# Kernel tuning notes

Hardware: AMD Instinct MI355X
Metric: run time of the kernel (lower is better)

## Reference

```python
import jax, jax.numpy as jnp
import numpy as np


def setup_inputs() -> dict:
    key = jax.random.key(0)
    k1, k2, k3, k4 = jax.random.split(key, 4)
    B, C, H, W = 8, 256, 64, 64
    x = jax.random.normal(k1, (B, C, H, W), dtype=jnp.float32)
    wq = jax.random.normal(k2, (1, C), dtype=jnp.float32) * (1.0 / np.sqrt(C))
    wk = jax.random.normal(k3, (1, C), dtype=jnp.float32) * (1.0 / np.sqrt(C))
    wv = jax.random.normal(k4, (C, C), dtype=jnp.float32) * (1.0 / np.sqrt(C))
    gamma = jnp.zeros((1,), dtype=jnp.float32)
    return {"x": x, "wq": wq, "wk": wk, "wv": wv, "gamma": gamma}


def reference(x, wq, wk, wv, gamma):
    B, C, H, W = x.shape
    N = H * W
    xf = x.reshape(B, C, N)                      # [B, C, N]
    # 1x1 convs == channel matmuls
    f = jnp.einsum('oc,bcn->bon', wq, xf)        # [B, 1, N]
    g = jnp.einsum('oc,bcn->bon', wk, xf)        # [B, 1, N]
    h = jnp.einsum('oc,bcn->bon', wv, xf)        # [B, C, N]
    # scores[b, i, j] = f[b, 0, i] * g[b, 0, j]  -> [B, N, N]
    scores = jnp.einsum('bi,bj->bij', f[:, 0, :], g[:, 0, :])
    # softmax over dim=1 (rows), matching torch F.softmax(..., dim=1)
    beta = jax.nn.softmax(scores, axis=1)        # [B, N, N]
    gam = gamma[0]
    o = (1.0 - gam) * jnp.einsum('bcn,bnm->bcm', h, beta) + gam * xf
    return o.reshape(B, C, H, W)
```

## Files before the change

### kernel.cpp

```cpp
#include <hip/hip_runtime.h>
#include <math.h>

#define BQ 8
#define CQ 256
#define NQ 4096
#define MT 128
#define NSTEP (NQ / 32)

typedef short s16x8 __attribute__((ext_vector_type(8)));
typedef short s16x4 __attribute__((ext_vector_type(4)));
typedef float f32x4 __attribute__((ext_vector_type(4)));

static __device__ __forceinline__ float4 ld4(const float* p) { return *(const float4*)p; }

static constexpr float LOG2E = 1.4426950408889634f;

static __device__ __forceinline__ short f2bf(float f) {
    return __builtin_bit_cast(short, (__bf16)f);
}

__global__ void k_fg(const float* __restrict__ x, const float* __restrict__ wq,
                     const float* __restrict__ wk, float* __restrict__ fs,
                     float* __restrict__ g, short* __restrict__ xbf) {
    int b = blockIdx.y;
    int n = blockIdx.x * 256 + threadIdx.x;
    const float* xb = x + (size_t)b * CQ * NQ + n;
    short* xo = xbf + (size_t)b * CQ * NQ + n;
    float accf = 0.f, accg = 0.f;
#pragma unroll 8
    for (int c = 0; c < CQ; ++c) {
        float v = xb[(size_t)c * NQ];
        accf = fmaf(wq[c], v, accf);
        accg = fmaf(wk[c], v, accg);
        xo[(size_t)c * NQ] = f2bf(v);
    }
    fs[b * NQ + n] = accf * LOG2E;
    g[b * NQ + n]  = accg;
}

__global__ void k_minmax(const float* __restrict__ fs, float* __restrict__ fmx,
                         float* __restrict__ fmn) {
    int b = blockIdx.x;
    const float* f = fs + b * NQ;
    float mx = -1e30f, mn = 1e30f;
    for (int i = threadIdx.x; i < NQ; i += 256) {
        float v = f[i];
        mx = fmaxf(mx, v);
        mn = fminf(mn, v);
    }
    for (int off = 32; off; off >>= 1) {
        mx = fmaxf(mx, __shfl_down(mx, off));
        mn = fminf(mn, __shfl_down(mn, off));
    }
    __shared__ float smx[4], smn[4];
    int wid = threadIdx.x >> 6;
    if ((threadIdx.x & 63) == 0) { smx[wid] = mx; smn[wid] = mn; }
    __syncthreads();
    if (threadIdx.x == 0) {
        mx = fmaxf(fmaxf(smx[0], smx[1]), fmaxf(smx[2], smx[3]));
        mn = fminf(fminf(smn[0], smn[1]), fminf(smn[2], smn[3]));
        fmx[b] = mx;
        fmn[b] = mn;
    }
}

__global__ void __launch_bounds__(512, 2) k_attn(
    const short* __restrict__ xbf, const float* __restrict__ fsp,
    const float* __restrict__ gp, const float* __restrict__ fmxs,
    const float* __restrict__ fmns, const float* __restrict__ wv,
    const float* __restrict__ x, const float* __restrict__ gamma,
    float* __restrict__ out) {
    __shared__ __align__(16) char smem[65536];

    int bid = blockIdx.x;
    int b = bid & 7;
    int mblk = bid >> 3;
    int m0 = mblk * MT;
    int tid = threadIdx.x;
    int l = tid & 63;
    int w = tid >> 6;
    int wc = w & 1;
    int wm = w >> 1;
    int q = l >> 4;
    int cr = l & 15;

    float fmx = fmxs[b], fmn = fmns[b];
    const float* gb = gp + b * NQ;
    float gj[2], nM[2], zac[2];
#pragma unroll
    for (int jm = 0; jm < 2; ++jm) {
        float gv = gb[m0 + wm * 32 + jm * 16 + cr];
        gj[jm] = gv;
        nM[jm] = -((gv >= 0.f) ? gv * fmx : gv * fmn);
        zac[jm] = 0.f;
    }

    const float* fb = fsp + b * NQ;
    const short* xb = xbf + (size_t)b * CQ * NQ;

    f32x4 acc[8][2];
#pragma unroll
    for (int jc = 0; jc < 8; ++jc)
#pragma unroll
        for (int jm = 0; jm < 2; ++jm) acc[jc][jm] = (f32x4){0.f, 0.f, 0.f, 0.f};

#pragma unroll
    for (int r2 = 0; r2 < 2; ++r2) {
        int off = tid * 16 + r2 * 8192;
        int row = off >> 6, nb = off & 63;
        const short* src = xb + (size_t)row * NQ + (nb >> 1);
        __builtin_amdgcn_global_load_lds(
            (const __attribute__((address_space(1))) void*)src,
            (__attribute__((address_space(3))) void*)(smem + off), 16, 0, 0);
    }
    float4 fqa = *(const float4*)(fb + q * 8);
    float4 fqb = *(const float4*)(fb + q * 8 + 4);
    __syncthreads();

    for (int t = 0; t < NSTEP; ++t) {
        const char* cbuf = smem + (t & 1) * 16384;
        int n0n = ((t + 1) & (NSTEP - 1)) * 32;
        if (t + 1 < NSTEP) {
            char* nbuf = smem + ((t + 1) & 1) * 16384;
#pragma unroll
            for (int r2 = 0; r2 < 2; ++r2) {
                int off = tid * 16 + r2 * 8192;
                int row = off >> 6, nb = off & 63;
                const short* src = xb + (size_t)row * NQ + n0n + (nb >> 1);
                __builtin_amdgcn_global_load_lds(
                    (const __attribute__((address_space(1))) void*)src,
                    (__attribute__((address_space(3))) void*)(nbuf + off), 16, 0, 0);
            }
        }
        float4 fqa_n = *(const float4*)(fb + n0n + q * 8);
        float4 fqb_n = *(const float4*)(fb + n0n + q * 8 + 4);
        float fq[8] = {fqa.x, fqa.y, fqa.z, fqa.w, fqb.x, fqb.y, fqb.z, fqb.w};
        s16x8 bv[2];
#pragma unroll
        for (int jm = 0; jm < 2; ++jm) {
            float z = zac[jm];
#pragma unroll
            for (int i = 0; i < 8; ++i) {
                float e = __builtin_amdgcn_exp2f(fmaf(fq[i], gj[jm], nM[jm]));
                z += e;
                bv[jm][i] = f2bf(e);
            }
            zac[jm] = z;
        }
#pragma unroll
        for (int jc = 0; jc < 8; ++jc) {
            s16x8 av = *(const s16x8*)(cbuf + (wc * 128 + jc * 16 + cr) * 64 + q * 16);
            acc[jc][0] = __builtin_amdgcn_mfma_f32_16x16x32_bf16(av, bv[0], acc[jc][0], 0, 0, 0);
            acc[jc][1] = __builtin_amdgcn_mfma_f32_16x16x32_bf16(av, bv[1], acc[jc][1], 0, 0, 0);
        }
        fqa = fqa_n;
        fqb = fqb_n;
        __syncthreads();
    }

    float rzl[2];
#pragma unroll
    for (int jm = 0; jm < 2; ++jm) {
        float z = zac[jm];
        z += __shfl_xor(z, 16);
        z += __shfl_xor(z, 32);
        rzl[jm] = 1.0f / z;
    }

#pragma unroll
    for (int jc = 0; jc < 8; ++jc) {
#pragma unroll
        for (int jm = 0; jm < 2; ++jm) {
            int mloc = wm * 32 + jm * 16 + cr;
            int bir = (wc * 256 + jc * 32 + q * 8) ^ ((mloc & 7) << 4);
            s16x4 v;
#pragma unroll
            for (int r = 0; r < 4; ++r) v[r] = f2bf(acc[jc][jm][r] * rzl[jm]);
            *(s16x4*)(smem + mloc * 512 + bir) = v;
        }
    }
    __syncthreads();

    int co0 = w * 32;
    f32x4 acc2[2][8];
#pragma unroll
    for (int j2 = 0; j2 < 2; ++j2)
#pragma unroll
        for (int jm2 = 0; jm2 < 8; ++jm2) acc2[j2][jm2] = (f32x4){0.f, 0.f, 0.f, 0.f};

#pragma unroll 2
    for (int ks = 0; ks < 8; ++ks) {
        s16x8 a2[2];
#pragma unroll
        for (int j2 = 0; j2 < 2; ++j2) {
            const float* wr = wv + (size_t)(co0 + j2 * 16 + cr) * CQ + ks * 32 + q * 8;
            float4 wa = ld4(wr);
            float4 wb = ld4(wr + 4);
            a2[j2][0] = f2bf(wa.x); a2[j2][1] = f2bf(wa.y);
            a2[j2][2] = f2bf(wa.z); a2[j2][3] = f2bf(wa.w);
            a2[j2][4] = f2bf(wb.x); a2[j2][5] = f2bf(wb.y);
            a2[j2][6] = f2bf(wb.z); a2[j2][7] = f2bf(wb.w);
        }
#pragma unroll
        for (int jm2 = 0; jm2 < 8; ++jm2) {
            int mloc = jm2 * 16 + cr;
            s16x8 b2 = *(const s16x8*)(smem + mloc * 512 + ((ks * 64 + q * 16) ^ ((mloc & 7) << 4)));
            acc2[0][jm2] = __builtin_amdgcn_mfma_f32_16x16x32_bf16(a2[0], b2, acc2[0][jm2], 0, 0, 0);
            acc2[1][jm2] = __builtin_amdgcn_mfma_f32_16x16x32_bf16(a2[1], b2, acc2[1][jm2], 0, 0, 0);
        }
    }

    float gam = gamma[0];
    float omg = 1.f - gam;
    if (gam != 0.f) {
#pragma unroll
        for (int j2 = 0; j2 < 2; ++j2)
#pragma unroll
            for (int jm2 = 0; jm2 < 8; ++jm2)
#pragma unroll
                for (int r = 0; r < 4; ++r) {
                    int c_out = co0 + j2 * 16 + q * 4 + r;
                    size_t idx = ((size_t)b * CQ + c_out) * NQ + m0 + jm2 * 16 + cr;
                    __builtin_nontemporal_store(
                        fmaf(gam, x[idx], acc2[j2][jm2][r] * omg), out + idx);
                }
    } else {
#pragma unroll
        for (int j2 = 0; j2 < 2; ++j2)
#pragma unroll
            for (int jm2 = 0; jm2 < 8; ++jm2)
#pragma unroll
                for (int r = 0; r < 4; ++r) {
                    int c_out = co0 + j2 * 16 + q * 4 + r;
                    size_t idx = ((size_t)b * CQ + c_out) * NQ + m0 + jm2 * 16 + cr;
                    __builtin_nontemporal_store(acc2[j2][jm2][r] * omg, out + idx);
                }
    }
}

extern "C" void kernel_launch(void* const* d_in, const int* in_sizes, int n_in,
                              void* d_out, int out_size, void* d_ws, size_t ws_size,
                              hipStream_t stream) {
    const float* x     = (const float*)d_in[0];
    const float* wq    = (const float*)d_in[1];
    const float* wk    = (const float*)d_in[2];
    const float* wv    = (const float*)d_in[3];
    const float* gamma = (const float*)d_in[4];
    float* out = (float*)d_out;

    float* ws  = (float*)d_ws;
    float* fs  = ws;
    float* g   = ws + BQ * NQ;
    float* fmx = ws + 2 * BQ * NQ;
    float* fmn = fmx + BQ;
    short* xbf = (short*)(ws + 2 * BQ * NQ + 64);

    hipLaunchKernelGGL(k_fg, dim3(NQ / 256, BQ), dim3(256), 0, stream, x, wq, wk, fs, g, xbf);
    hipLaunchKernelGGL(k_minmax, dim3(BQ), dim3(256), 0, stream, fs, fmx, fmn);
    hipLaunchKernelGGL(k_attn, dim3(BQ * (NQ / MT)), dim3(512), 0, stream,
                       xbf, fs, g, fmx, fmn, wv, x, gamma, out);
}
```

Before: 129.9 us.

## Widen per-wave attention tile to 256 threads and split k_fg channel reduction

k_attn now runs with 256 threads instead of 512. Each wave covers 64 query columns instead of 32, so every LDS A-fragment feeds four MFMAs instead of two, and the output projection computes 64 channels per wave. k_fg splits the 256-channel reduction across four wave groups and combines the partial sums through shared memory, so it launches four times as many blocks and fills the GPU better. The cost is fewer resident waves for hiding latency in k_attn, much higher accumulator register pressure, and an extra shared-memory sync in k_fg.

Result: slower. 135.8 us (+4.6%).

```diff
diff --git a/kernel.cpp b/kernel.cpp
--- a/kernel.cpp
+++ b/kernel.cpp
@@ -23,19 +23,30 @@
                      const float* __restrict__ wk, float* __restrict__ fs,
                      float* __restrict__ g, short* __restrict__ xbf) {
     int b = blockIdx.y;
-    int n = blockIdx.x * 256 + threadIdx.x;
+    int nloc = threadIdx.x & 63;
+    int cg = threadIdx.x >> 6;
+    int n = blockIdx.x * 64 + nloc;
     const float* xb = x + (size_t)b * CQ * NQ + n;
     short* xo = xbf + (size_t)b * CQ * NQ + n;
     float accf = 0.f, accg = 0.f;
+    int c0 = cg * 64;
 #pragma unroll 8
-    for (int c = 0; c < CQ; ++c) {
+    for (int c = c0; c < c0 + 64; ++c) {
         float v = xb[(size_t)c * NQ];
         accf = fmaf(wq[c], v, accf);
         accg = fmaf(wk[c], v, accg);
         xo[(size_t)c * NQ] = f2bf(v);
     }
-    fs[b * NQ + n] = accf * LOG2E;
-    g[b * NQ + n]  = accg;
+    __shared__ float sf[4][64], sg2[4][64];
+    sf[cg][nloc] = accf;
+    sg2[cg][nloc] = accg;
+    __syncthreads();
+    if (threadIdx.x < 64) {
+        float f = sf[0][nloc] + sf[1][nloc] + sf[2][nloc] + sf[3][nloc];
+        float gg = sg2[0][nloc] + sg2[1][nloc] + sg2[2][nloc] + sg2[3][nloc];
+        fs[b * NQ + blockIdx.x * 64 + nloc] = f * LOG2E;
+        g[b * NQ + blockIdx.x * 64 + nloc] = gg;
+    }
 }
 
 __global__ void k_minmax(const float* __restrict__ fs, float* __restrict__ fmx,
@@ -64,7 +75,7 @@
     }
 }
 
-__global__ void __launch_bounds__(512, 2) k_attn(
+__global__ void __launch_bounds__(256, 2) k_attn(
     const short* __restrict__ xbf, const float* __restrict__ fsp,
     const float* __restrict__ gp, const float* __restrict__ fmxs,
     const float* __restrict__ fmns, const float* __restrict__ wv,
@@ -86,10 +97,10 @@
 
     float fmx = fmxs[b], fmn = fmns[b];
     const float* gb = gp + b * NQ;
-    float gj[2], nM[2], zac[2];
-#pragma unroll
-    for (int jm = 0; jm < 2; ++jm) {
-        float gv = gb[m0 + wm * 32 + jm * 16 + cr];
+    float gj[4], nM[4], zac[4];
+#pragma unroll
+    for (int jm = 0; jm < 4; ++jm) {
+        float gv = gb[m0 + wm * 64 + jm * 16 + cr];
         gj[jm] = gv;
         nM[jm] = -((gv >= 0.f) ? gv * fmx : gv * fmn);
         zac[jm] = 0.f;
@@ -98,15 +109,15 @@
     const float* fb = fsp + b * NQ;
     const short* xb = xbf + (size_t)b * CQ * NQ;
 
-    f32x4 acc[8][2];
+    f32x4 acc[8][4];
 #pragma unroll
     for (int jc = 0; jc < 8; ++jc)
 #pragma unroll
-        for (int jm = 0; jm < 2; ++jm) acc[jc][jm] = (f32x4){0.f, 0.f, 0.f, 0.f};
-
-#pragma unroll
-    for (int r2 = 0; r2 < 2; ++r2) {
-        int off = tid * 16 + r2 * 8192;
+        for (int jm = 0; jm < 4; ++jm) acc[jc][jm] = (f32x4){0.f, 0.f, 0.f, 0.f};
+
+#pragma unroll
+    for (int r2 = 0; r2 < 4; ++r2) {
+        int off = tid * 16 + r2 * 4096;
         int row = off >> 6, nb = off & 63;
         const short* src = xb + (size_t)row * NQ + (nb >> 1);
         __builtin_amdgcn_global_load_lds(
@@ -123,8 +134,8 @@
         if (t + 1 < NSTEP) {
             char* nbuf = smem + ((t + 1) & 1) * 16384;
 #pragma unroll
-            for (int r2 = 0; r2 < 2; ++r2) {
-                int off = tid * 16 + r2 * 8192;
+            for (int r2 = 0; r2 < 4; ++r2) {
+                int off = tid * 16 + r2 * 4096;
                 int row = off >> 6, nb = off & 63;
                 const short* src = xb + (size_t)row * NQ + n0n + (nb >> 1);
                 __builtin_amdgcn_global_load_lds(
@@ -135,9 +146,9 @@
         float4 fqa_n = *(const float4*)(fb + n0n + q * 8);
         float4 fqb_n = *(const float4*)(fb + n0n + q * 8 + 4);
         float fq[8] = {fqa.x, fqa.y, fqa.z, fqa.w, fqb.x, fqb.y, fqb.z, fqb.w};
-        s16x8 bv[2];
-#pragma unroll
-        for (int jm = 0; jm < 2; ++jm) {
+        s16x8 bv[4];
+#pragma unroll
+        for (int jm = 0; jm < 4; ++jm) {
             float z = zac[jm];
 #pragma unroll
             for (int i = 0; i < 8; ++i) {
@@ -150,17 +161,18 @@
 #pragma unroll
         for (int jc = 0; jc < 8; ++jc) {
             s16x8 av = *(const s16x8*)(cbuf + (wc * 128 + jc * 16 + cr) * 64 + q * 16);
-            acc[jc][0] = __builtin_amdgcn_mfma_f32_16x16x32_bf16(av, bv[0], acc[jc][0], 0, 0, 0);
-            acc[jc][1] = __builtin_amdgcn_mfma_f32_16x16x32_bf16(av, bv[1], acc[jc][1], 0, 0, 0);
+#pragma unroll
+            for (int jm = 0; jm < 4; ++jm)
+                acc[jc][jm] = __builtin_amdgcn_mfma_f32_16x16x32_bf16(av, bv[jm], acc[jc][jm], 0, 0, 0);
         }
         fqa = fqa_n;
         fqb = fqb_n;
         __syncthreads();
     }
 
-    float rzl[2];
-#pragma unroll
-    for (int jm = 0; jm < 2; ++jm) {
+    float rzl[4];
+#pragma unroll
+    for (int jm = 0; jm < 4; ++jm) {
         float z = zac[jm];
         z += __shfl_xor(z, 16);
         z += __shfl_xor(z, 32);
@@ -170,29 +182,29 @@
 #pragma unroll
     for (int jc = 0; jc < 8; ++jc) {
 #pragma unroll
-        for (int jm = 0; jm < 2; ++jm) {
-            int mloc = wm * 32 + jm * 16 + cr;
-            int bir = (wc * 256 + jc * 32 + q * 8) ^ ((mloc & 7) << 4);
+        for (int jm = 0; jm < 4; ++jm) {
+            int mloc = wm * 64 + jm * 16 + cr;
+            int cb = (wc * 256 + jc * 32 + q * 8) ^ ((mloc & 7) << 4);
             s16x4 v;
 #pragma unroll
             for (int r = 0; r < 4; ++r) v[r] = f2bf(acc[jc][jm][r] * rzl[jm]);
-            *(s16x4*)(smem + mloc * 512 + bir) = v;
-        }
-    }
-    __syncthreads();
-
-    int co0 = w * 32;
-    f32x4 acc2[2][8];
-#pragma unroll
-    for (int j2 = 0; j2 < 2; ++j2)
+            *(s16x4*)(smem + mloc * 512 + cb) = v;
+        }
+    }
+    __syncthreads();
+
+    int co0 = w * 64;
+    f32x4 acc2[4][8];
+#pragma unroll
+    for (int j2 = 0; j2 < 4; ++j2)
 #pragma unroll
         for (int jm2 = 0; jm2 < 8; ++jm2) acc2[j2][jm2] = (f32x4){0.f, 0.f, 0.f, 0.f};
 
 #pragma unroll 2
     for (int ks = 0; ks < 8; ++ks) {
-        s16x8 a2[2];
-#pragma unroll
-        for (int j2 = 0; j2 < 2; ++j2) {
+        s16x8 a2[4];
+#pragma unroll
+        for (int j2 = 0; j2 < 4; ++j2) {
             const float* wr = wv + (size_t)(co0 + j2 * 16 + cr) * CQ + ks * 32 + q * 8;
             float4 wa = ld4(wr);
             float4 wb = ld4(wr + 4);
@@ -205,8 +217,9 @@
         for (int jm2 = 0; jm2 < 8; ++jm2) {
             int mloc = jm2 * 16 + cr;
             s16x8 b2 = *(const s16x8*)(smem + mloc * 512 + ((ks * 64 + q * 16) ^ ((mloc & 7) << 4)));
-            acc2[0][jm2] = __builtin_amdgcn_mfma_f32_16x16x32_bf16(a2[0], b2, acc2[0][jm2], 0, 0, 0);
-            acc2[1][jm2] = __builtin_amdgcn_mfma_f32_16x16x32_bf16(a2[1], b2, acc2[1][jm2], 0, 0, 0);
+#pragma unroll
+            for (int j2 = 0; j2 < 4; ++j2)
+                acc2[j2][jm2] = __builtin_amdgcn_mfma_f32_16x16x32_bf16(a2[j2], b2, acc2[j2][jm2], 0, 0, 0);
         }
     }
 
@@ -214,7 +227,7 @@
     float omg = 1.f - gam;
     if (gam != 0.f) {
 #pragma unroll
-        for (int j2 = 0; j2 < 2; ++j2)
+        for (int j2 = 0; j2 < 4; ++j2)
 #pragma unroll
             for (int jm2 = 0; jm2 < 8; ++jm2)
 #pragma unroll
@@ -226,7 +239,7 @@
                 }
     } else {
 #pragma unroll
-        for (int j2 = 0; j2 < 2; ++j2)
+        for (int j2 = 0; j2 < 4; ++j2)
 #pragma unroll
             for (int jm2 = 0; jm2 < 8; ++jm2)
 #pragma unroll
@@ -255,8 +268,8 @@
     float* fmn = fmx + BQ;
     short* xbf = (short*)(ws + 2 * BQ * NQ + 64);
 
-    hipLaunchKernelGGL(k_fg, dim3(NQ / 256, BQ), dim3(256), 0, stream, x, wq, wk, fs, g, xbf);
+    hipLaunchKernelGGL(k_fg, dim3(NQ / 64, BQ), dim3(256), 0, stream, x, wq, wk, fs, g, xbf);
     hipLaunchKernelGGL(k_minmax, dim3(BQ), dim3(256), 0, stream, fs, fmx, fmn);
-    hipLaunchKernelGGL(k_attn, dim3(BQ * (NQ / MT)), dim3(512), 0, stream,
+    hipLaunchKernelGGL(k_attn, dim3(BQ * (NQ / MT)), dim3(256), 0, stream,
                        xbf, fs, g, fmx, fmn, wv, x, gamma, out);
 }
```
